# Performance work log

Measured on AMD Instinct MI355X. Metric: run time of the kernel, lower is better.

The kernel has to match this reference:

```python
import jax, jax.numpy as jnp
import numpy as np
import math

IN_DIM = 3
WIDTH = 256
DEPTH = 6
OUT_DIM = 1
W0_FIRST = 30.0
W0_HIDDEN = 1.0
N_POINTS = 1048576


def _uniform(key, shape, bound):
    return jax.random.uniform(key, shape, dtype=jnp.float32, minval=-bound, maxval=bound)


def setup_inputs() -> dict:
    key = jax.random.key(0)
    ks = jax.random.split(key, 8)
    xyt = jax.random.uniform(ks[0], (N_POINTS, IN_DIM), dtype=jnp.float32, minval=-1.0, maxval=1.0)
    # first layer: bound = 1/in_features
    W0 = _uniform(ks[1], (WIDTH, IN_DIM), 1.0 / IN_DIM)
    b0 = jnp.zeros((WIDTH,), jnp.float32)
    # hidden layers: bound = sqrt(6/width)/w0_hidden
    hb = math.sqrt(6.0 / WIDTH) / W0_HIDDEN
    W1 = _uniform(ks[2], (WIDTH, WIDTH), hb)
    b1 = jnp.zeros((WIDTH,), jnp.float32)
    W2 = _uniform(ks[3], (WIDTH, WIDTH), hb)
    b2 = jnp.zeros((WIDTH,), jnp.float32)
    W3 = _uniform(ks[4], (WIDTH, WIDTH), hb)
    b3 = jnp.zeros((WIDTH,), jnp.float32)
    W4 = _uniform(ks[5], (WIDTH, WIDTH), hb)
    b4 = jnp.zeros((WIDTH,), jnp.float32)
    Wf = _uniform(ks[6], (OUT_DIM, WIDTH), hb)
    bf = jnp.zeros((OUT_DIM,), jnp.float32)
    return {"xyt": xyt, "W0": W0, "b0": b0, "W1": W1, "b1": b1,
            "W2": W2, "b2": b2, "W3": W3, "b3": b3, "W4": W4, "b4": b4,
            "Wf": Wf, "bf": bf}


def reference(xyt, W0, b0, W1, b1, W2, b2, W3, b3, W4, b4, Wf, bf):
    # SineLayer: sin(w0 * (x @ W^T + b)); torch Linear weight is [out, in]
    h = jnp.sin(W0_FIRST * (xyt @ W0.T + b0))          # [N, 256]
    for W, b in ((W1, b1), (W2, b2), (W3, b3), (W4, b4)):
        h = jnp.sin(W0_HIDDEN * (h @ W.T + b))          # [N, 256]
    out = h @ Wf.T + bf                                  # [N, 1]
    return out.squeeze(-1)                               # [N]
```

## Files before the change

kernel.cpp:

```cpp
#include <hip/hip_runtime.h>

typedef _Float16 half8 __attribute__((ext_vector_type(8)));
typedef _Float16 half4 __attribute__((ext_vector_type(4)));
typedef float f32x4 __attribute__((ext_vector_type(4)));

#define NPB 128
#define THREADS 512
#define INV2PI 0.15915494309189535f
#define W0SCALE (30.0f * INV2PI)
#define SMEM_BYTES (NPB * 256 * 2 + (384 + 256) * 4)

__device__ __forceinline__ int hswz(int row, int col) {
    return (row << 8) + (col ^ ((row & 7) << 3));
}

__global__ void convert_weights(const float* __restrict__ W1, const float* __restrict__ W2,
                                const float* __restrict__ W3, const float* __restrict__ W4,
                                _Float16* __restrict__ Wc) {
    int tid = blockIdx.x * 256 + threadIdx.x;
    int l   = tid >> 16;
    int rem = tid & 65535;
    int n = rem >> 8, k = rem & 255;
    const float* W = (l == 0) ? W1 : (l == 1) ? W2 : (l == 2) ? W3 : W4;
    int kc = k >> 5, kl = k & 31;
    Wc[l * 65536 + kc * 8192 + n * 32 + kl] = (_Float16)(W[rem] * INV2PI);
}

__launch_bounds__(THREADS, 4)
__global__ void siren_fused(const float* __restrict__ xyt,
                            const float* __restrict__ W0,
                            const float* __restrict__ b0,
                            const _Float16* __restrict__ Wc,
                            const float* __restrict__ b1,
                            const float* __restrict__ b2,
                            const float* __restrict__ b3,
                            const float* __restrict__ b4,
                            const float* __restrict__ Wf,
                            const float* __restrict__ bfin,
                            float* __restrict__ out)
{
    extern __shared__ _Float16 smem[];
    _Float16* hbuf = smem;
    float* xs   = (float*)(smem + NPB * 256);
    float* wf_s = xs + 384;

    const int tid  = threadIdx.x;
    const int lane = tid & 63;
    const int wv   = tid >> 6;
    const int l15  = lane & 15;
    const int l4   = lane >> 4;
    const int gm0  = blockIdx.x * NPB;

    if (tid < 384) xs[tid] = xyt[gm0 * 3 + tid];
    if (tid < 256) wf_s[tid] = Wf[tid];
    __syncthreads();

    {
        const int fg = lane;
        const int p0 = wv * 16;
        float w[4][3], bb[4];
        #pragma unroll
        for (int c = 0; c < 4; ++c) {
            const int n = fg * 4 + c;
            w[c][0] = W0[n * 3 + 0] * W0SCALE;
            w[c][1] = W0[n * 3 + 1] * W0SCALE;
            w[c][2] = W0[n * 3 + 2] * W0SCALE;
            bb[c]   = b0[n] * W0SCALE;
        }
        #pragma unroll 4
        for (int p = 0; p < 16; ++p) {
            const float x0 = xs[(p0 + p) * 3], x1 = xs[(p0 + p) * 3 + 1], x2 = xs[(p0 + p) * 3 + 2];
            half4 hv;
            #pragma unroll
            for (int c = 0; c < 4; ++c) {
                float z = fmaf(w[c][0], x0, fmaf(w[c][1], x1, fmaf(w[c][2], x2, bb[c])));
                hv[c] = (_Float16)__builtin_amdgcn_sinf(z);
            }
            *(half4*)&hbuf[hswz(p0 + p, fg * 4)] = hv;
        }
    }

    const int arow = (wv * 32 + l15) * 32 + l4 * 8;

    #pragma unroll
    for (int l = 0; l < 4; ++l) {
        const float* bl = (l == 0) ? b1 : (l == 1) ? b2 : (l == 2) ? b3 : b4;
        const _Float16* wl = Wc + l * 65536;

        half8 areg[2][2];
        #pragma unroll
        for (int c = 0; c < 2; ++c)
            #pragma unroll
            for (int i = 0; i < 2; ++i)
                areg[c][i] = *(const half8*)&wl[c * 8192 + arow + i * 512];

        f32x4 acc[2][8];
        #pragma unroll
        for (int i = 0; i < 2; ++i) {
            f32x4 bb = *(const f32x4*)&bl[wv * 32 + i * 16 + l4 * 4];
            bb *= INV2PI;
            #pragma unroll
            for (int j = 0; j < 8; ++j)
                acc[i][j] = bb;
        }

        __syncthreads();

        #pragma unroll
        for (int kc = 0; kc < 8; ++kc) {
            half8 anext[2];
            if (kc < 6) {
                #pragma unroll
                for (int i = 0; i < 2; ++i)
                    anext[i] = *(const half8*)&wl[(kc + 2) * 8192 + arow + i * 512];
            }
            #pragma unroll
            for (int g = 0; g < 2; ++g) {
                half8 bfr[4];
                #pragma unroll
                for (int j = 0; j < 4; ++j)
                    bfr[j] = *(const half8*)&hbuf[hswz((g * 4 + j) * 16 + l15, kc * 32 + l4 * 8)];
                #pragma unroll
                for (int i = 0; i < 2; ++i)
                    #pragma unroll
                    for (int j = 0; j < 4; ++j)
                        acc[i][g * 4 + j] = __builtin_amdgcn_mfma_f32_16x16x32_f16(
                            areg[kc & 1][i], bfr[j], acc[i][g * 4 + j], 0, 0, 0);
            }
            if (kc < 6) { areg[kc & 1][0] = anext[0]; areg[kc & 1][1] = anext[1]; }
        }

        __syncthreads();

        #pragma unroll
        for (int i = 0; i < 2; ++i)
            #pragma unroll
            for (int j = 0; j < 8; ++j) {
                half4 hv;
                #pragma unroll
                for (int r = 0; r < 4; ++r)
                    hv[r] = (_Float16)__builtin_amdgcn_sinf(acc[i][j][r]);
                *(half4*)&hbuf[hswz(j * 16 + l15, wv * 32 + i * 16 + l4 * 4)] = hv;
            }
    }

    __syncthreads();

    {
        const int m = tid >> 2, q = tid & 3;
        float sum = 0.f;
        #pragma unroll
        for (int i = 0; i < 8; ++i) {
            half8 hv = *(const half8*)&hbuf[hswz(m, q * 64 + i * 8)];
            const int nb = q * 64 + i * 8;
            #pragma unroll
            for (int j = 0; j < 8; ++j)
                sum = fmaf((float)hv[j], wf_s[nb + j], sum);
        }
        sum += __shfl_down(sum, 2);
        sum += __shfl_down(sum, 1);
        if (q == 0) out[gm0 + m] = sum + bfin[0];
    }
}

extern "C" void kernel_launch(void* const* d_in, const int* in_sizes, int n_in,
                              void* d_out, int out_size, void* d_ws, size_t ws_size,
                              hipStream_t stream) {
    const float* xyt = (const float*)d_in[0];
    const float* W0  = (const float*)d_in[1];
    const float* b0  = (const float*)d_in[2];
    const float* W1  = (const float*)d_in[3];
    const float* b1  = (const float*)d_in[4];
    const float* W2  = (const float*)d_in[5];
    const float* b2  = (const float*)d_in[6];
    const float* W3  = (const float*)d_in[7];
    const float* b3  = (const float*)d_in[8];
    const float* W4  = (const float*)d_in[9];
    const float* b4  = (const float*)d_in[10];
    const float* Wf  = (const float*)d_in[11];
    const float* bf  = (const float*)d_in[12];
    float* out = (float*)d_out;
    _Float16* Wc = (_Float16*)d_ws;

    hipFuncSetAttribute((const void*)siren_fused,
                        hipFuncAttributeMaxDynamicSharedMemorySize, SMEM_BYTES);

    convert_weights<<<1024, 256, 0, stream>>>(W1, W2, W3, W4, Wc);

    const int N = in_sizes[0] / 3;
    siren_fused<<<N / NPB, THREADS, SMEM_BYTES, stream>>>(
        xyt, W0, b0, Wc, b1, b2, b3, b4, Wf, bf, out);
}
```

Baseline: 606.2 us.

## Retile per-wave MFMA work to 64x64 blocks and compute sine before barrier

Each wave now covers a 64-feature by 64-point tile instead of 32 features by all 128 points. This halves the LDS activation fragments loaded per wave and doubles the weight fragments read from global memory. The double-buffered weight prefetch is removed in favor of loading four A fragments per k-chunk. The sine evaluation is moved ahead of the barrier so it can overlap with other waves still doing MFMA, at the cost of holding 16 half4 values in registers.

```diff
diff --git a/kernel.cpp b/kernel.cpp
--- a/kernel.cpp
+++ b/kernel.cpp
@@ -47,6 +47,8 @@
     const int tid  = threadIdx.x;
     const int lane = tid & 63;
     const int wv   = tid >> 6;
+    const int pg   = wv >> 2;
+    const int fb   = (wv & 3) << 6;
     const int l15  = lane & 15;
     const int l4   = lane >> 4;
     const int gm0  = blockIdx.x * NPB;
@@ -80,27 +82,20 @@
         }
     }
 
-    const int arow = (wv * 32 + l15) * 32 + l4 * 8;
+    const int arow = (fb + l15) * 32 + l4 * 8;
 
     #pragma unroll
     for (int l = 0; l < 4; ++l) {
         const float* bl = (l == 0) ? b1 : (l == 1) ? b2 : (l == 2) ? b3 : b4;
         const _Float16* wl = Wc + l * 65536;
 
-        half8 areg[2][2];
+        f32x4 acc[4][4];
         #pragma unroll
-        for (int c = 0; c < 2; ++c)
-            #pragma unroll
-            for (int i = 0; i < 2; ++i)
-                areg[c][i] = *(const half8*)&wl[c * 8192 + arow + i * 512];
-
-        f32x4 acc[2][8];
-        #pragma unroll
-        for (int i = 0; i < 2; ++i) {
-            f32x4 bb = *(const f32x4*)&bl[wv * 32 + i * 16 + l4 * 4];
+        for (int i = 0; i < 4; ++i) {
+            f32x4 bb = *(const f32x4*)&bl[fb + i * 16 + l4 * 4];
             bb *= INV2PI;
             #pragma unroll
-            for (int j = 0; j < 8; ++j)
+            for (int j = 0; j < 4; ++j)
                 acc[i][j] = bb;
         }
 
@@ -108,40 +103,42 @@
 
         #pragma unroll
         for (int kc = 0; kc < 8; ++kc) {
-            half8 anext[2];
-            if (kc < 6) {
-                #pragma unroll
-                for (int i = 0; i < 2; ++i)
-                    anext[i] = *(const half8*)&wl[(kc + 2) * 8192 + arow + i * 512];
-            }
+            half8 a[4];
+            #pragma unroll
+            for (int i = 0; i < 4; ++i)
+                a[i] = *(const half8*)&wl[kc * 8192 + arow + i * 512];
             #pragma unroll
             for (int g = 0; g < 2; ++g) {
-                half8 bfr[4];
+                half8 bfr[2];
                 #pragma unroll
-                for (int j = 0; j < 4; ++j)
-                    bfr[j] = *(const half8*)&hbuf[hswz((g * 4 + j) * 16 + l15, kc * 32 + l4 * 8)];
+                for (int j = 0; j < 2; ++j)
+                    bfr[j] = *(const half8*)&hbuf[hswz(pg * 64 + (g * 2 + j) * 16 + l15,
+                                                       kc * 32 + l4 * 8)];
                 #pragma unroll
-                for (int i = 0; i < 2; ++i)
+                for (int i = 0; i < 4; ++i)
                     #pragma unroll
-                    for (int j = 0; j < 4; ++j)
-                        acc[i][g * 4 + j] = __builtin_amdgcn_mfma_f32_16x16x32_f16(
-                            areg[kc & 1][i], bfr[j], acc[i][g * 4 + j], 0, 0, 0);
+                    for (int j = 0; j < 2; ++j)
+                        acc[i][g * 2 + j] = __builtin_amdgcn_mfma_f32_16x16x32_f16(
+                            a[i], bfr[j], acc[i][g * 2 + j], 0, 0, 0);
             }
-            if (kc < 6) { areg[kc & 1][0] = anext[0]; areg[kc & 1][1] = anext[1]; }
         }
+
+        half4 hv[4][4];
+        #pragma unroll
+        for (int i = 0; i < 4; ++i)
+            #pragma unroll
+            for (int j = 0; j < 4; ++j)
+                #pragma unroll
+                for (int r = 0; r < 4; ++r)
+                    hv[i][j][r] = (_Float16)__builtin_amdgcn_sinf(acc[i][j][r]);
 
         __syncthreads();
 
         #pragma unroll
-        for (int i = 0; i < 2; ++i)
+        for (int i = 0; i < 4; ++i)
             #pragma unroll
-            for (int j = 0; j < 8; ++j) {
-                half4 hv;
-                #pragma unroll
-                for (int r = 0; r < 4; ++r)
-                    hv[r] = (_Float16)__builtin_amdgcn_sinf(acc[i][j][r]);
-                *(half4*)&hbuf[hswz(j * 16 + l15, wv * 32 + i * 16 + l4 * 4)] = hv;
-            }
+            for (int j = 0; j < 4; ++j)
+                *(half4*)&hbuf[hswz(pg * 64 + j * 16 + l15, fb + i * 16 + l4 * 4)] = hv[i][j];
     }
 
     __syncthreads();
```

After: 708.2 us. 1.17x slower.
